# Kernel optimization log

Hardware: AMD Instinct MI355X
Metric: run time of the kernel (lower is better)

## Reference

```python
import jax, jax.numpy as jnp
import numpy as np

N_QUBITS = 2
Q_DEPTH = 2
B = 2_097_152


def _rot(phi, theta, omega):
    """PennyLane Rot gate: RZ(omega) @ RY(theta) @ RZ(phi), shape [2,2] complex."""
    ct = jnp.cos(theta * 0.5)
    st = jnp.sin(theta * 0.5)
    m00 = jnp.exp(-0.5j * (phi + omega)) * ct
    m01 = -jnp.exp(0.5j * (phi - omega)) * st
    m10 = jnp.exp(-0.5j * (phi - omega)) * st
    m11 = jnp.exp(0.5j * (phi + omega)) * ct
    return jnp.stack([jnp.stack([m00, m01]), jnp.stack([m10, m11])])


def _circuit(noise, q_weights):
    # AngleEmbedding (RX rotations) applied to |00>: state = RX(a0)|0> (x) RX(a1)|0>
    angles = noise.astype(jnp.float32) * jnp.pi  # original: rand * pi
    c = jnp.cos(angles * 0.5)                    # [B,2]
    s = jnp.sin(angles * 0.5)
    v0 = jnp.stack([c[:, 0] + 0j, -1j * s[:, 0]], axis=1)  # [B,2] amps of qubit 0
    v1 = jnp.stack([c[:, 1] + 0j, -1j * s[:, 1]], axis=1)  # [B,2] amps of qubit 1
    state = v0[:, :, None] * v1[:, None, :]                # [B,2,2] statevector

    # StronglyEntanglingLayers: per layer Rot on each wire, then CNOT ring (r=1)
    for l in range(Q_DEPTH):
        g0 = _rot(q_weights[l, 0, 0], q_weights[l, 0, 1], q_weights[l, 0, 2])
        g1 = _rot(q_weights[l, 1, 0], q_weights[l, 1, 1], q_weights[l, 1, 2])
        state = jnp.einsum('ij,bjk->bik', g0, state)  # gate on qubit 0
        state = jnp.einsum('ij,bkj->bki', g1, state)  # gate on qubit 1
        # CNOT(control=0, target=1): flip qubit-1 index where qubit-0 == 1
        state = jnp.stack([state[:, 0, :], state[:, 1, ::-1]], axis=1)
        # CNOT(control=1, target=0): flip qubit-0 index where qubit-1 == 1
        state = jnp.stack([state[:, :, 0], state[:, ::-1, 1]], axis=2)

    probs = jnp.abs(state) ** 2  # [B,2,2]
    z0 = probs[:, 0, :].sum(-1) - probs[:, 1, :].sum(-1)  # <Z> on wire 0
    z1 = probs[:, :, 0].sum(-1) - probs[:, :, 1].sum(-1)  # <Z> on wire 1
    return jnp.stack([z0, z1], axis=1).astype(jnp.float32)  # [B,2]


def setup_inputs() -> dict:
    key = jax.random.key(0)
    k1, k2 = jax.random.split(key)
    noise = jax.random.uniform(k1, (B, N_QUBITS), dtype=jnp.float32)
    q_weights = 0.1 * jax.random.normal(k2, (Q_DEPTH, N_QUBITS, 3), dtype=jnp.float32)
    return {"noise": noise, "q_weights": q_weights}


def reference(noise, q_weights):
    return _circuit(noise, q_weights)
```

## Files before the change

kernel.cpp:

```cpp
#include <hip/hip_runtime.h>
#include <math.h>


struct Cx { float re, im; };
__device__ inline Cx cmul(Cx a, Cx b){ return {a.re*b.re - a.im*b.im, a.re*b.im + a.im*b.re}; }
__device__ inline Cx cmadd2(Cx a, Cx x, Cx b, Cx y){
  Cx p = cmul(a,x), q = cmul(b,y);
  return { p.re + q.re, p.im + q.im };
}

__device__ inline float quadform(const float* __restrict__ A,
                                 float r0, float r1, float r2, float r3) {
  float t0 = A[0]*r0  + A[1]*r1  + A[2]*r2  + A[3]*r3;
  float t1 = A[4]*r0  + A[5]*r1  + A[6]*r2  + A[7]*r3;
  float t2 = A[8]*r0  + A[9]*r1  + A[10]*r2 + A[11]*r3;
  float t3 = A[12]*r0 + A[13]*r1 + A[14]*r2 + A[15]*r3;
  return r0*t0 + r1*t1 + r2*t2 + r3*t3;
}

__global__ __launch_bounds__(256) void qc_kernel(const float* __restrict__ noise,
                                                 const float* __restrict__ w,
                                                 float* __restrict__ out,
                                                 int nQuads) {
  __shared__ float sA[32];

  if (threadIdx.x == 0) {
    Cx U[4][4];
    for (int r = 0; r < 4; ++r)
      for (int c = 0; c < 4; ++c)
        U[r][c] = { (r == c) ? 1.f : 0.f, 0.f };

    for (int l = 0; l < 2; ++l) {
      Cx g[2][2][2];
      for (int q = 0; q < 2; ++q) {
        float phi = w[l*6 + q*3 + 0];
        float th  = w[l*6 + q*3 + 1];
        float om  = w[l*6 + q*3 + 2];
        float st, ct; sincosf(0.5f*th, &st, &ct);
        float sp, cp; sincosf(0.5f*(phi+om), &sp, &cp);
        float sm, cm; sincosf(0.5f*(phi-om), &sm, &cm);
        g[q][0][0] = {  cp*ct, -sp*ct };
        g[q][0][1] = { -cm*st, -sm*st };
        g[q][1][0] = {  cm*st, -sm*st };
        g[q][1][1] = {  cp*ct,  sp*ct };
      }
      for (int c = 0; c < 4; ++c)
        for (int k = 0; k < 2; ++k) {
          Cx x0 = U[k][c], x1 = U[2+k][c];
          U[k][c]   = cmadd2(g[0][0][0], x0, g[0][0][1], x1);
          U[2+k][c] = cmadd2(g[0][1][0], x0, g[0][1][1], x1);
        }
      for (int c = 0; c < 4; ++c)
        for (int j = 0; j < 2; ++j) {
          Cx x0 = U[2*j][c], x1 = U[2*j+1][c];
          U[2*j][c]   = cmadd2(g[1][0][0], x0, g[1][0][1], x1);
          U[2*j+1][c] = cmadd2(g[1][1][0], x0, g[1][1][1], x1);
        }
      for (int c = 0; c < 4; ++c) { Cx t = U[2][c]; U[2][c] = U[3][c]; U[3][c] = t; }
      for (int c = 0; c < 4; ++c) { Cx t = U[1][c]; U[1][c] = U[3][c]; U[3][c] = t; }
    }

    for (int r = 0; r < 4; ++r) {
      Cx t;
      t = U[r][1]; U[r][1] = {  t.im, -t.re };
      t = U[r][2]; U[r][2] = {  t.im, -t.re };
      t = U[r][3]; U[r][3] = { -t.re, -t.im };
    }

    const float z0s[4] = { 1.f,  1.f, -1.f, -1.f };
    const float z1s[4] = { 1.f, -1.f,  1.f, -1.f };
    for (int a = 0; a < 4; ++a)
      for (int b = 0; b < 4; ++b) {
        float a0 = 0.f, a1 = 0.f;
        for (int r = 0; r < 4; ++r) {
          float d = U[r][a].re*U[r][b].re + U[r][a].im*U[r][b].im;
          a0 += z0s[r]*d;
          a1 += z1s[r]*d;
        }
        sA[a*4 + b]      = a0;
        sA[16 + a*4 + b] = a1;
      }
  }
  __syncthreads();

  float A0[16], A1[16];
  #pragma unroll
  for (int i = 0; i < 16; ++i) { A0[i] = sA[i]; A1[i] = sA[16 + i]; }

  const float4* __restrict__ in4  = (const float4*)noise;
  float4* __restrict__ out4 = (float4*)out;
  const float HPI = 1.57079632679489662f;

  int gid    = blockIdx.x * blockDim.x + threadIdx.x;
  int stride = gridDim.x * blockDim.x;
  for (int i = gid; i < nQuads; i += stride) {
    float4 v = in4[i];
    float4 o;
    {
      float s0, c0, s1, c1;
      __sincosf(v.x * HPI, &s0, &c0);
      __sincosf(v.y * HPI, &s1, &c1);
      float r0 = c0*c1, r1 = c0*s1, r2 = s0*c1, r3 = s0*s1;
      o.x = quadform(A0, r0, r1, r2, r3);
      o.y = quadform(A1, r0, r1, r2, r3);
    }
    {
      float s0, c0, s1, c1;
      __sincosf(v.z * HPI, &s0, &c0);
      __sincosf(v.w * HPI, &s1, &c1);
      float r0 = c0*c1, r1 = c0*s1, r2 = s0*c1, r3 = s0*s1;
      o.z = quadform(A0, r0, r1, r2, r3);
      o.w = quadform(A1, r0, r1, r2, r3);
    }
    out4[i] = o;
  }
}

extern "C" void kernel_launch(void* const* d_in, const int* in_sizes, int n_in,
                              void* d_out, int out_size, void* d_ws, size_t ws_size,
                              hipStream_t stream) {
  const float* noise = (const float*)d_in[0];
  const float* w     = (const float*)d_in[1];
  float* out         = (float*)d_out;

  int nQuads = in_sizes[0] / 4;
  int threads = 256;
  int blocks  = 1024;
  qc_kernel<<<blocks, threads, 0, stream>>>(noise, w, out, nQuads);
}
```

Measured before the change: 74.79 us.

## Precompute reduced trig-basis coefficients in a prep kernel and simplify per-element evaluation

The per-block serial unitary build moves into a separate single-thread prep kernel that writes a 3x3 coefficient matrix per output to workspace. The 4x4 quadratic form in half-angle products is rewritten as a bilinear form in cos/sin of the full angle, which cuts per-element FMAs. The main kernel now uses one thread per quad with a full grid instead of a grid-stride loop. The cost is an extra kernel launch and a dependency through global memory.

```diff
diff --git a/kernel.cpp b/kernel.cpp
--- a/kernel.cpp
+++ b/kernel.cpp
@@ -9,111 +9,134 @@
   return { p.re + q.re, p.im + q.im };
 }
 
-__device__ inline float quadform(const float* __restrict__ A,
-                                 float r0, float r1, float r2, float r3) {
-  float t0 = A[0]*r0  + A[1]*r1  + A[2]*r2  + A[3]*r3;
-  float t1 = A[4]*r0  + A[5]*r1  + A[6]*r2  + A[7]*r3;
-  float t2 = A[8]*r0  + A[9]*r1  + A[10]*r2 + A[11]*r3;
-  float t3 = A[12]*r0 + A[13]*r1 + A[14]*r2 + A[15]*r3;
-  return r0*t0 + r1*t1 + r2*t2 + r3*t3;
+__global__ void qc_prep(const float* __restrict__ w, float* __restrict__ K) {
+  if (threadIdx.x != 0) return;
+
+  Cx U[4][4];
+  for (int r = 0; r < 4; ++r)
+    for (int c = 0; c < 4; ++c)
+      U[r][c] = { (r == c) ? 1.f : 0.f, 0.f };
+
+  for (int l = 0; l < 2; ++l) {
+    Cx g[2][2][2];
+    for (int q = 0; q < 2; ++q) {
+      float phi = w[l*6 + q*3 + 0];
+      float th  = w[l*6 + q*3 + 1];
+      float om  = w[l*6 + q*3 + 2];
+      float st, ct; sincosf(0.5f*th, &st, &ct);
+      float sp, cp; sincosf(0.5f*(phi+om), &sp, &cp);
+      float sm, cm; sincosf(0.5f*(phi-om), &sm, &cm);
+      g[q][0][0] = {  cp*ct, -sp*ct };
+      g[q][0][1] = { -cm*st, -sm*st };
+      g[q][1][0] = {  cm*st, -sm*st };
+      g[q][1][1] = {  cp*ct,  sp*ct };
+    }
+    for (int c = 0; c < 4; ++c)
+      for (int k = 0; k < 2; ++k) {
+        Cx x0 = U[k][c], x1 = U[2+k][c];
+        U[k][c]   = cmadd2(g[0][0][0], x0, g[0][0][1], x1);
+        U[2+k][c] = cmadd2(g[0][1][0], x0, g[0][1][1], x1);
+      }
+    for (int c = 0; c < 4; ++c)
+      for (int j = 0; j < 2; ++j) {
+        Cx x0 = U[2*j][c], x1 = U[2*j+1][c];
+        U[2*j][c]   = cmadd2(g[1][0][0], x0, g[1][0][1], x1);
+        U[2*j+1][c] = cmadd2(g[1][1][0], x0, g[1][1][1], x1);
+      }
+    for (int c = 0; c < 4; ++c) { Cx t = U[2][c]; U[2][c] = U[3][c]; U[3][c] = t; }
+    for (int c = 0; c < 4; ++c) { Cx t = U[1][c]; U[1][c] = U[3][c]; U[3][c] = t; }
+  }
+
+  for (int r = 0; r < 4; ++r) {
+    Cx t;
+    t = U[r][1]; U[r][1] = {  t.im, -t.re };
+    t = U[r][2]; U[r][2] = {  t.im, -t.re };
+    t = U[r][3]; U[r][3] = { -t.re, -t.im };
+  }
+
+  const float z0s[4] = { 1.f,  1.f, -1.f, -1.f };
+  const float z1s[4] = { 1.f, -1.f,  1.f, -1.f };
+  float A[2][16];
+  for (int a = 0; a < 4; ++a)
+    for (int b = 0; b < 4; ++b) {
+      float a0 = 0.f, a1 = 0.f;
+      for (int r = 0; r < 4; ++r) {
+        float d = U[r][a].re*U[r][b].re + U[r][a].im*U[r][b].im;
+        a0 += z0s[r]*d;
+        a1 += z1s[r]*d;
+      }
+      A[0][a*4 + b] = a0;
+      A[1][a*4 + b] = a1;
+    }
+
+  float M[2][9];
+  for (int q = 0; q < 2; ++q) {
+    const float* a = A[q];
+    M[q][0] = a[0];
+    M[q][1] = 2.f*a[1];
+    M[q][2] = a[5];
+    M[q][3] = 2.f*a[2];
+    M[q][4] = 2.f*(a[3]+a[6]);
+    M[q][5] = 2.f*a[7];
+    M[q][6] = a[10];
+    M[q][7] = 2.f*a[11];
+    M[q][8] = a[15];
+  }
+
+  const float T[3][3] = { {0.5f, 0.5f, 0.f},
+                          {0.f,  0.f,  0.5f},
+                          {0.5f, -0.5f, 0.f} };
+  for (int q = 0; q < 2; ++q)
+    for (int c = 0; c < 3; ++c)
+      for (int d = 0; d < 3; ++d) {
+        float acc = 0.f;
+        for (int a = 0; a < 3; ++a)
+          for (int b = 0; b < 3; ++b)
+            acc += T[a][c] * M[q][a*3+b] * T[b][d];
+        K[q*9 + c*3 + d] = acc;
+      }
 }
 
-__global__ __launch_bounds__(256) void qc_kernel(const float* __restrict__ noise,
-                                                 const float* __restrict__ w,
-                                                 float* __restrict__ out,
-                                                 int nQuads) {
-  __shared__ float sA[32];
+__device__ inline float evalK(const float* __restrict__ k,
+                              float C0, float S0, float C1, float S1) {
+  float t0 = fmaf(k[2], S1, fmaf(k[1], C1, k[0]));
+  float t1 = fmaf(k[5], S1, fmaf(k[4], C1, k[3]));
+  float t2 = fmaf(k[8], S1, fmaf(k[7], C1, k[6]));
+  return fmaf(S0, t2, fmaf(C0, t1, t0));
+}
 
-  if (threadIdx.x == 0) {
-    Cx U[4][4];
-    for (int r = 0; r < 4; ++r)
-      for (int c = 0; c < 4; ++c)
-        U[r][c] = { (r == c) ? 1.f : 0.f, 0.f };
+__global__ __launch_bounds__(256) void qc_main(const float* __restrict__ noise,
+                                               const float* __restrict__ Kg,
+                                               float* __restrict__ out,
+                                               int nQuads) {
+  float k0[9], k1[9];
+  #pragma unroll
+  for (int i = 0; i < 9; ++i) { k0[i] = Kg[i]; k1[i] = Kg[9 + i]; }
 
-    for (int l = 0; l < 2; ++l) {
-      Cx g[2][2][2];
-      for (int q = 0; q < 2; ++q) {
-        float phi = w[l*6 + q*3 + 0];
-        float th  = w[l*6 + q*3 + 1];
-        float om  = w[l*6 + q*3 + 2];
-        float st, ct; sincosf(0.5f*th, &st, &ct);
-        float sp, cp; sincosf(0.5f*(phi+om), &sp, &cp);
-        float sm, cm; sincosf(0.5f*(phi-om), &sm, &cm);
-        g[q][0][0] = {  cp*ct, -sp*ct };
-        g[q][0][1] = { -cm*st, -sm*st };
-        g[q][1][0] = {  cm*st, -sm*st };
-        g[q][1][1] = {  cp*ct,  sp*ct };
-      }
-      for (int c = 0; c < 4; ++c)
-        for (int k = 0; k < 2; ++k) {
-          Cx x0 = U[k][c], x1 = U[2+k][c];
-          U[k][c]   = cmadd2(g[0][0][0], x0, g[0][0][1], x1);
-          U[2+k][c] = cmadd2(g[0][1][0], x0, g[0][1][1], x1);
-        }
-      for (int c = 0; c < 4; ++c)
-        for (int j = 0; j < 2; ++j) {
-          Cx x0 = U[2*j][c], x1 = U[2*j+1][c];
-          U[2*j][c]   = cmadd2(g[1][0][0], x0, g[1][0][1], x1);
-          U[2*j+1][c] = cmadd2(g[1][1][0], x0, g[1][1][1], x1);
-        }
-      for (int c = 0; c < 4; ++c) { Cx t = U[2][c]; U[2][c] = U[3][c]; U[3][c] = t; }
-      for (int c = 0; c < 4; ++c) { Cx t = U[1][c]; U[1][c] = U[3][c]; U[3][c] = t; }
-    }
-
-    for (int r = 0; r < 4; ++r) {
-      Cx t;
-      t = U[r][1]; U[r][1] = {  t.im, -t.re };
-      t = U[r][2]; U[r][2] = {  t.im, -t.re };
-      t = U[r][3]; U[r][3] = { -t.re, -t.im };
-    }
-
-    const float z0s[4] = { 1.f,  1.f, -1.f, -1.f };
-    const float z1s[4] = { 1.f, -1.f,  1.f, -1.f };
-    for (int a = 0; a < 4; ++a)
-      for (int b = 0; b < 4; ++b) {
-        float a0 = 0.f, a1 = 0.f;
-        for (int r = 0; r < 4; ++r) {
-          float d = U[r][a].re*U[r][b].re + U[r][a].im*U[r][b].im;
-          a0 += z0s[r]*d;
-          a1 += z1s[r]*d;
-        }
-        sA[a*4 + b]      = a0;
-        sA[16 + a*4 + b] = a1;
-      }
-  }
-  __syncthreads();
-
-  float A0[16], A1[16];
-  #pragma unroll
-  for (int i = 0; i < 16; ++i) { A0[i] = sA[i]; A1[i] = sA[16 + i]; }
-
+  const float PI = 3.14159265358979323846f;
   const float4* __restrict__ in4  = (const float4*)noise;
   float4* __restrict__ out4 = (float4*)out;
-  const float HPI = 1.57079632679489662f;
 
-  int gid    = blockIdx.x * blockDim.x + threadIdx.x;
-  int stride = gridDim.x * blockDim.x;
-  for (int i = gid; i < nQuads; i += stride) {
-    float4 v = in4[i];
-    float4 o;
-    {
-      float s0, c0, s1, c1;
-      __sincosf(v.x * HPI, &s0, &c0);
-      __sincosf(v.y * HPI, &s1, &c1);
-      float r0 = c0*c1, r1 = c0*s1, r2 = s0*c1, r3 = s0*s1;
-      o.x = quadform(A0, r0, r1, r2, r3);
-      o.y = quadform(A1, r0, r1, r2, r3);
-    }
-    {
-      float s0, c0, s1, c1;
-      __sincosf(v.z * HPI, &s0, &c0);
-      __sincosf(v.w * HPI, &s1, &c1);
-      float r0 = c0*c1, r1 = c0*s1, r2 = s0*c1, r3 = s0*s1;
-      o.z = quadform(A0, r0, r1, r2, r3);
-      o.w = quadform(A1, r0, r1, r2, r3);
-    }
-    out4[i] = o;
+  int i = blockIdx.x * blockDim.x + threadIdx.x;
+  if (i >= nQuads) return;
+
+  float4 v = in4[i];
+  float4 o;
+  {
+    float S0, C0, S1, C1;
+    __sincosf(v.x * PI, &S0, &C0);
+    __sincosf(v.y * PI, &S1, &C1);
+    o.x = evalK(k0, C0, S0, C1, S1);
+    o.y = evalK(k1, C0, S0, C1, S1);
   }
+  {
+    float S0, C0, S1, C1;
+    __sincosf(v.z * PI, &S0, &C0);
+    __sincosf(v.w * PI, &S1, &C1);
+    o.z = evalK(k0, C0, S0, C1, S1);
+    o.w = evalK(k1, C0, S0, C1, S1);
+  }
+  out4[i] = o;
 }
 
 extern "C" void kernel_launch(void* const* d_in, const int* in_sizes, int n_in,
@@ -122,9 +145,12 @@
   const float* noise = (const float*)d_in[0];
   const float* w     = (const float*)d_in[1];
   float* out         = (float*)d_out;
+  float* K           = (float*)d_ws;
 
-  int nQuads = in_sizes[0] / 4;
+  qc_prep<<<1, 64, 0, stream>>>(w, K);
+
+  int nQuads  = in_sizes[0] / 4;
   int threads = 256;
-  int blocks  = 1024;
-  qc_kernel<<<blocks, threads, 0, stream>>>(noise, w, out, nQuads);
+  int blocks  = (nQuads + threads - 1) / threads;
+  qc_main<<<blocks, threads, 0, stream>>>(noise, K, out, nQuads);
 }
```

Result: no change. 73.60 us (-1.6%).
